# Kernel optimization log

Hardware: AMD Instinct MI355X
Metric: run time of the kernel (lower is better)

The kernel has to match this reference:

```python
import jax, jax.numpy as jnp
import numpy as np

B, C, H, W, R = 4, 128, 64, 256, 8  # batch, channels, height, width, window radius


def setup_inputs() -> dict:
    key = jax.random.key(0)
    k0, k1, k2, k3 = jax.random.split(key, 4)
    feature = jax.random.normal(k0, (B, C, H, W), dtype=jnp.float32)
    position = 0.02 * jax.random.normal(k1, (B, C, H, W), dtype=jnp.float32)
    # 1x1 conv weights (xavier-like scale), bias zeros as in nn.Conv2d default-ish
    Wq = jax.random.normal(k2, (C, C), dtype=jnp.float32) / np.float32(np.sqrt(C))
    Wk = jax.random.normal(k3, (C, C), dtype=jnp.float32) / np.float32(np.sqrt(C))
    bq = jnp.zeros((C,), dtype=jnp.float32)
    bk = jnp.zeros((C,), dtype=jnp.float32)
    return {"feature": feature, "position": position, "Wq": Wq, "bq": bq, "Wk": Wk, "bk": bk}


def reference(feature, position, Wq, bq, Wk, bk):
    # feature/position: [b, c, h, w]
    f = feature + position
    b, c, h, w = f.shape
    # 1x1 convs == channel matmuls
    q = jnp.einsum('oc,bchw->bohw', Wq, f) + bq[None, :, None, None]
    k = jnp.einsum('oc,bchw->bohw', Wk, f) + bk[None, :, None, None]
    r = R
    Kw = 2 * r + 1
    # pad along width, gather sliding windows: [b, c, h, w, Kw]
    kp = jnp.pad(k, ((0, 0), (0, 0), (0, 0), (r, r)))
    vp = jnp.pad(f, ((0, 0), (0, 0), (0, 0), (r, r)))
    idx = jnp.arange(w)[:, None] + jnp.arange(Kw)[None, :]  # [w, Kw]
    kwin = kp[:, :, :, idx]
    vwin = vp[:, :, :, idx]
    scale = jnp.asarray(np.sqrt(c), dtype=q.dtype)
    scores = jnp.einsum('bchw,bchwk->bhwk', q, kwin) / scale  # [b, h, w, Kw]
    attn = jax.nn.softmax(scores, axis=-1)
    out = jnp.einsum('bhwk,bchwk->bchw', attn, vwin)
    return out
```

## Files before the change

kernel.cpp:

```cpp
#include <hip/hip_runtime.h>
#include <hip/hip_bf16.h>
#include <math.h>

#define BB 4
#define CCH 128
#define HH 64
#define WW 256
#define RR 8
#define KWIN 17
#define TW 32
#define TWH 48
#define NTHREADS 256
#define PIT 136
#define FAP 48
#define PTP 48
#define PT_HI 5440
#define MROWS 144

typedef __attribute__((ext_vector_type(8))) short short8;
typedef __attribute__((ext_vector_type(4))) short short4v;
typedef __attribute__((ext_vector_type(4))) float f32x4;

__device__ __forceinline__ short f2bf(float x) {
    union { __hip_bfloat16 b; short s; } u;
    u.b = __float2bfloat16(x);
    return u.s;
}

__global__ __launch_bounds__(128)
void prep_kernel(const float* __restrict__ Wq, const float* __restrict__ bq,
                 const float* __restrict__ Wk, short* __restrict__ Mp)
{
    const int r = blockIdx.x;
    const int c = threadIdx.x;
    float acc = 0.f;
    if (r < CCH) {
        #pragma unroll 4
        for (int j = 0; j < CCH; ++j)
            acc = fmaf(Wq[j * CCH + r], Wk[j * CCH + c], acc);
    } else if (r == CCH) {
        #pragma unroll 4
        for (int o = 0; o < CCH; ++o)
            acc = fmaf(bq[o], Wk[o * CCH + c], acc);
    }
    Mp[r * CCH + c] = f2bf(acc);
}

#define ST_IDX(r) (((r) >> 4) * 1088 + ((r) & 15) * 36)

__global__ __launch_bounds__(NTHREADS, 4)
void attn1d_fused(const float* __restrict__ feature,
                  const float* __restrict__ position,
                  const short* __restrict__ Mp,
                  float* __restrict__ out)
{
    __shared__ __align__(16) char uA[TWH * PIT * 2];
    __shared__ __align__(16) char uB[TWH * PIT * 2];
    __shared__ __align__(16) short fA[CCH][FAP];
    __shared__ float ubias[TWH];
    short (*fBt)[PIT] = (short(*)[PIT])uA;
    short (*gT)[PIT]  = (short(*)[PIT])uB;
    float* Stp        = (float*)uB;
    short* uAs        = (short*)uA;

    const int t    = threadIdx.x;
    const int wid  = t >> 6;
    const int lane = t & 63;
    const int lrow = lane & 15;
    const int lgrp = lane >> 4;

    int blk = blockIdx.x;
    blk = (blk & 7) * 256 + (blk >> 3);
    const int wt = blk & 7;
    const int bh = blk >> 3;
    const int h  = bh & (HH - 1);
    const int b  = bh >> 6;
    const int w0 = wt * TW - RR;
    const int base = ((b * CCH) * HH + h) * WW;

    const int mrow = wid * 32;
    short8 Mf[2][4];
    #pragma unroll
    for (int mf = 0; mf < 2; ++mf)
        #pragma unroll
        for (int kk = 0; kk < 4; ++kk)
            Mf[mf][kk] = *(const short8*)(Mp + (mrow + mf * 16 + lrow) * CCH
                                             + kk * 32 + lgrp * 8);
    short8 Mf2[4];
    if (wid == 3) {
        #pragma unroll
        for (int kk = 0; kk < 4; ++kk)
            Mf2[kk] = *(const short8*)(Mp + (CCH + lrow) * CCH + kk * 32 + lgrp * 8);
    }

    #pragma unroll
    for (int i = 0; i < 6; ++i) {
        const int idx = i * NTHREADS + t;
        const int c  = idx / 12;
        const int wq = idx - c * 12;
        const int w  = w0 + wq * 4;
        float4 fv = {0.f, 0.f, 0.f, 0.f};
        if (w >= 0 && w < WW) {
            const int off = base + c * (HH * WW) + w;
            const float4 fa = *(const float4*)(feature + off);
            const float4 pa = *(const float4*)(position + off);
            fv.x = fa.x + pa.x; fv.y = fa.y + pa.y;
            fv.z = fa.z + pa.z; fv.w = fa.w + pa.w;
        }
        short4v s4;
        s4[0] = f2bf(fv.x); s4[1] = f2bf(fv.y); s4[2] = f2bf(fv.z); s4[3] = f2bf(fv.w);
        *(short4v*)&fA[c][wq * 4] = s4;
        fBt[wq * 4 + 0][c] = s4[0];
        fBt[wq * 4 + 1][c] = s4[1];
        fBt[wq * 4 + 2][c] = s4[2];
        fBt[wq * 4 + 3][c] = s4[3];
    }
    __syncthreads();

    {
        f32x4 acc[2][3];
        #pragma unroll
        for (int mf = 0; mf < 2; ++mf)
            #pragma unroll
            for (int nf = 0; nf < 3; ++nf)
                acc[mf][nf] = (f32x4){0.f, 0.f, 0.f, 0.f};
        f32x4 acc2[3];
        #pragma unroll
        for (int nf = 0; nf < 3; ++nf) acc2[nf] = (f32x4){0.f, 0.f, 0.f, 0.f};

        #pragma unroll
        for (int kk = 0; kk < 4; ++kk) {
            short8 bfr[3];
            #pragma unroll
            for (int nf = 0; nf < 3; ++nf)
                bfr[nf] = *(const short8*)&fBt[nf * 16 + lrow][kk * 32 + lgrp * 8];
            #pragma unroll
            for (int mf = 0; mf < 2; ++mf)
                #pragma unroll
                for (int nf = 0; nf < 3; ++nf)
                    acc[mf][nf] = __builtin_amdgcn_mfma_f32_16x16x32_bf16(
                        Mf[mf][kk], bfr[nf], acc[mf][nf], 0, 0, 0);
            if (wid == 3) {
                #pragma unroll
                for (int nf = 0; nf < 3; ++nf)
                    acc2[nf] = __builtin_amdgcn_mfma_f32_16x16x32_bf16(
                        Mf2[kk], bfr[nf], acc2[nf], 0, 0, 0);
            }
        }

        #pragma unroll
        for (int mf = 0; mf < 2; ++mf)
            #pragma unroll
            for (int nf = 0; nf < 3; ++nf) {
                short4v s;
                #pragma unroll
                for (int reg = 0; reg < 4; ++reg)
                    s[reg] = f2bf(acc[mf][nf][reg]);
                *(short4v*)&gT[nf * 16 + lrow][mrow + mf * 16 + lgrp * 4] = s;
            }
        if (wid == 3 && lgrp == 0) {
            const float isc = 0.08838834764831845f;
            #pragma unroll
            for (int nf = 0; nf < 3; ++nf)
                ubias[nf * 16 + lrow] = acc2[nf][0] * isc;
        }
    }
    __syncthreads();

    if (wid < 3) {
        const int nf = wid;
        f32x4 s0 = {0.f,0.f,0.f,0.f}, s1 = {0.f,0.f,0.f,0.f};
        #pragma unroll
        for (int kk = 0; kk < 4; ++kk) {
            const short8 a0 = *(const short8*)&fBt[RR + lrow     ][kk * 32 + lgrp * 8];
            const short8 a1 = *(const short8*)&fBt[RR + 16 + lrow][kk * 32 + lgrp * 8];
            const short8 bb = *(const short8*)&gT[nf * 16 + lrow][kk * 32 + lgrp * 8];
            s0 = __builtin_amdgcn_mfma_f32_16x16x32_bf16(a0, bb, s0, 0, 0, 0);
            s1 = __builtin_amdgcn_mfma_f32_16x16x32_bf16(a1, bb, s1, 0, 0, 0);
        }
        const float isc = 0.08838834764831845f;
        const int sb = ST_IDX(nf * 16 + lrow);
        *(f32x4*)&Stp[sb + lgrp * 4]      = s0 * isc;
        *(f32x4*)&Stp[sb + 16 + lgrp * 4] = s1 * isc;
    } else {
        const short8 z = {0,0,0,0,0,0,0,0};
        #pragma unroll
        for (int i = 0; i < 2; ++i) {
            const int q8 = i * 64 + lane;
            if (q8 < 96) {
                *(short8*)(uAs + q8 * 8) = z;
                *(short8*)(uAs + PT_HI + q8 * 8) = z;
            }
        }
    }
    __syncthreads();

    if (t < TW * 4) {
        const int w = t >> 2, g = t & 3;
        const int nt = (g == 0) ? 5 : 4;
        const int prow = (w < 16) ? (w * PTP) : (PT_HI + (w - 16) * PTP);
        float sv[5];
        float mx = -3.0e38f;
        #pragma unroll
        for (int i = 0; i < 5; ++i) {
            if (i < nt) {
                const int j = (i == 4) ? 16 : (g + i * 4);
                const int r = w + j;
                sv[i] = Stp[ST_IDX(r) + w] + ubias[r];
                mx = fmaxf(mx, sv[i]);
            }
        }
        mx = fmaxf(mx, __shfl_xor(mx, 1, 4));
        mx = fmaxf(mx, __shfl_xor(mx, 2, 4));
        float sum = 0.f;
        #pragma unroll
        for (int i = 0; i < 5; ++i)
            if (i < nt) { sv[i] = __expf(sv[i] - mx); sum += sv[i]; }
        sum += __shfl_xor(sum, 1, 4);
        sum += __shfl_xor(sum, 2, 4);
        const float inv = 1.f / sum;
        #pragma unroll
        for (int i = 0; i < 5; ++i)
            if (i < nt) {
                const int j = (i == 4) ? 16 : (g + i * 4);
                uAs[prow + w + j] = f2bf(sv[i] * inv);
            }
    }
    __syncthreads();

    {
        const int cb = wid * 32;
        const short8 z = {0,0,0,0,0,0,0,0};
        f32x4 d00 = {0.f,0.f,0.f,0.f}, d01 = d00, d10 = d00, d11 = d00;
        #pragma unroll
        for (int kk = 0; kk < 2; ++kk) {
            const int koff = kk * 32 + lgrp * 8;
            const bool live = (koff < TWH);
            short8 a0 = z, a1 = z, b0 = z, b1 = z;
            if (live) {
                a0 = *(const short8*)&fA[cb + lrow     ][koff];
                a1 = *(const short8*)&fA[cb + 16 + lrow][koff];
                b0 = *(const short8*)(uAs + lrow * PTP + koff);
                b1 = *(const short8*)(uAs + PT_HI + lrow * PTP + koff);
            }
            d00 = __builtin_amdgcn_mfma_f32_16x16x32_bf16(a0, b0, d00, 0, 0, 0);
            d01 = __builtin_amdgcn_mfma_f32_16x16x32_bf16(a0, b1, d01, 0, 0, 0);
            d10 = __builtin_amdgcn_mfma_f32_16x16x32_bf16(a1, b0, d10, 0, 0, 0);
            d11 = __builtin_amdgcn_mfma_f32_16x16x32_bf16(a1, b1, d11, 0, 0, 0);
        }
        const int wbase = wt * TW;
        #pragma unroll
        for (int reg = 0; reg < 4; ++reg) {
            const int c0 = cb + lgrp * 4 + reg;
            out[base + c0 * (HH * WW)        + wbase + lrow]      = d00[reg];
            out[base + c0 * (HH * WW)        + wbase + 16 + lrow] = d01[reg];
            out[base + (c0 + 16) * (HH * WW) + wbase + lrow]      = d10[reg];
            out[base + (c0 + 16) * (HH * WW) + wbase + 16 + lrow] = d11[reg];
        }
    }
}

extern "C" void kernel_launch(void* const* d_in, const int* in_sizes, int n_in,
                              void* d_out, int out_size, void* d_ws, size_t ws_size,
                              hipStream_t stream) {
    const float* feature  = (const float*)d_in[0];
    const float* position = (const float*)d_in[1];
    const float* Wq = (const float*)d_in[2];
    const float* bq = (const float*)d_in[3];
    const float* Wk = (const float*)d_in[4];
    const float* bk = (const float*)d_in[5];
    (void)bk;
    float* out = (float*)d_out;
    short* Mp  = (short*)d_ws;

    prep_kernel<<<MROWS, 128, 0, stream>>>(Wq, bq, Wk, Mp);
    const dim3 grid(BB * HH * (WW / TW));
    attn1d_fused<<<grid, NTHREADS, 0, stream>>>(feature, position, Mp, out);
}
```

Baseline: 40.11 us.

## Split fused attention into transform and attention kernels via bf16 workspace

Splits the single fused kernel into two. The first converts feature+position to bf16, computes the projected keys (M·f) and the bias term once per position, and writes transposed and normal copies to a global workspace. The second kernel does the windowed scores, softmax and output matmul by reading those bf16 tensors. This removes the halo recomputation of the projection and halves the bytes read by the attention stage. In exchange it adds a full round trip of several bf16 intermediate tensors through global memory plus one more kernel launch. The old fused kernel is kept as a fallback for when the workspace is too small.

```diff
diff --git a/kernel.cpp b/kernel.cpp
--- a/kernel.cpp
+++ b/kernel.cpp
@@ -12,10 +12,16 @@
 #define TWH 48
 #define NTHREADS 256
 #define PIT 136
-#define FAP 48
-#define PTP 48
-#define PT_HI 5440
+#define STP 36
+#define PTP 56
 #define MROWS 144
+
+#define SZ_BHWC (BB * HH * WW * CCH * 2)
+#define OFF_FT  65536
+#define OFF_GT  (OFF_FT + SZ_BHWC)
+#define OFF_FN  (OFF_GT + SZ_BHWC)
+#define OFF_UB  (OFF_FN + SZ_BHWC)
+#define WS_NEED ((size_t)OFF_UB + (size_t)(BB * HH * WW * 4))
 
 typedef __attribute__((ext_vector_type(8))) short short8;
 typedef __attribute__((ext_vector_type(4))) short short4v;
@@ -46,6 +52,252 @@
     Mp[r * CCH + c] = f2bf(acc);
 }
 
+__global__ __launch_bounds__(NTHREADS, 4)
+void k1_transform(const float* __restrict__ feature,
+                  const float* __restrict__ position,
+                  const short* __restrict__ Mp,
+                  short* __restrict__ fTg, short* __restrict__ gTg,
+                  short* __restrict__ fNg, float* __restrict__ ubg)
+{
+    __shared__ __align__(16) short fBt[64][PIT];
+
+    const int t    = threadIdx.x;
+    const int wid  = t >> 6;
+    const int lane = t & 63;
+    const int lrow = lane & 15;
+    const int lgrp = lane >> 4;
+
+    int blk = blockIdx.x;
+    blk = (blk & 7) * 128 + (blk >> 3);
+    const int wt = blk & 3;
+    const int bh = blk >> 2;
+    const int h  = bh & (HH - 1);
+    const int b  = bh >> 6;
+    const int w0 = wt * 64;
+    const int base = ((b * CCH) * HH + h) * WW;
+    const int bhw  = (b * HH + h) * WW;
+
+    const int mrow = wid * 32;
+    short8 Mf[2][4];
+    #pragma unroll
+    for (int mf = 0; mf < 2; ++mf)
+        #pragma unroll
+        for (int kk = 0; kk < 4; ++kk)
+            Mf[mf][kk] = *(const short8*)(Mp + (mrow + mf * 16 + lrow) * CCH
+                                             + kk * 32 + lgrp * 8);
+    short8 Mf2[4];
+    if (wid == 3) {
+        #pragma unroll
+        for (int kk = 0; kk < 4; ++kk)
+            Mf2[kk] = *(const short8*)(Mp + (CCH + lrow) * CCH + kk * 32 + lgrp * 8);
+    }
+
+    #pragma unroll
+    for (int i = 0; i < 8; ++i) {
+        const int idx = i * NTHREADS + t;
+        const int c  = idx >> 4;
+        const int wq = idx & 15;
+        const int off = base + c * (HH * WW) + w0 + wq * 4;
+        const float4 fa = *(const float4*)(feature + off);
+        const float4 pa = *(const float4*)(position + off);
+        short4v s4;
+        s4[0] = f2bf(fa.x + pa.x); s4[1] = f2bf(fa.y + pa.y);
+        s4[2] = f2bf(fa.z + pa.z); s4[3] = f2bf(fa.w + pa.w);
+        fBt[wq * 4 + 0][c] = s4[0];
+        fBt[wq * 4 + 1][c] = s4[1];
+        fBt[wq * 4 + 2][c] = s4[2];
+        fBt[wq * 4 + 3][c] = s4[3];
+        *(short4v*)(fNg + ((b * CCH + c) * HH + h) * WW + w0 + wq * 4) = s4;
+    }
+    __syncthreads();
+
+    {
+        const int r  = t >> 2;
+        const int ch = (t & 3) * 32;
+        short* dst = fTg + (bhw + w0 + r) * CCH + ch;
+        #pragma unroll
+        for (int q = 0; q < 4; ++q)
+            *(short8*)(dst + q * 8) = *(const short8*)&fBt[r][ch + q * 8];
+    }
+
+    f32x4 acc[2][4];
+    #pragma unroll
+    for (int mf = 0; mf < 2; ++mf)
+        #pragma unroll
+        for (int nf = 0; nf < 4; ++nf)
+            acc[mf][nf] = (f32x4){0.f, 0.f, 0.f, 0.f};
+    f32x4 acc2[4];
+    #pragma unroll
+    for (int nf = 0; nf < 4; ++nf) acc2[nf] = (f32x4){0.f, 0.f, 0.f, 0.f};
+
+    #pragma unroll
+    for (int kk = 0; kk < 4; ++kk) {
+        short8 bfr[4];
+        #pragma unroll
+        for (int nf = 0; nf < 4; ++nf)
+            bfr[nf] = *(const short8*)&fBt[nf * 16 + lrow][kk * 32 + lgrp * 8];
+        #pragma unroll
+        for (int mf = 0; mf < 2; ++mf)
+            #pragma unroll
+            for (int nf = 0; nf < 4; ++nf)
+                acc[mf][nf] = __builtin_amdgcn_mfma_f32_16x16x32_bf16(
+                    Mf[mf][kk], bfr[nf], acc[mf][nf], 0, 0, 0);
+        if (wid == 3) {
+            #pragma unroll
+            for (int nf = 0; nf < 4; ++nf)
+                acc2[nf] = __builtin_amdgcn_mfma_f32_16x16x32_bf16(
+                    Mf2[kk], bfr[nf], acc2[nf], 0, 0, 0);
+        }
+    }
+
+    #pragma unroll
+    for (int mf = 0; mf < 2; ++mf)
+        #pragma unroll
+        for (int nf = 0; nf < 4; ++nf) {
+            short4v s;
+            #pragma unroll
+            for (int reg = 0; reg < 4; ++reg)
+                s[reg] = f2bf(acc[mf][nf][reg]);
+            *(short4v*)(gTg + (bhw + w0 + nf * 16 + lrow) * CCH
+                            + mrow + mf * 16 + lgrp * 4) = s;
+        }
+    if (wid == 3 && lgrp == 0) {
+        const float isc = 0.08838834764831845f;
+        #pragma unroll
+        for (int nf = 0; nf < 4; ++nf)
+            ubg[bhw + w0 + nf * 16 + lrow] = acc2[nf][0] * isc;
+    }
+}
+
+__global__ __launch_bounds__(NTHREADS, 8)
+void k2_attn(const short* __restrict__ fTg, const short* __restrict__ gTg,
+             const short* __restrict__ fNg, const float* __restrict__ ubg,
+             float* __restrict__ out)
+{
+    __shared__ __align__(16) float St[TWH][STP];
+    __shared__ __align__(16) short Pt[33][PTP];
+    __shared__ float ubl[TWH];
+
+    const int t    = threadIdx.x;
+    const int wid  = t >> 6;
+    const int lane = t & 63;
+    const int lrow = lane & 15;
+    const int lgrp = lane >> 4;
+
+    int blk = blockIdx.x;
+    blk = (blk & 7) * 256 + (blk >> 3);
+    const int wt = blk & 7;
+    const int bh = blk >> 3;
+    const int h  = bh & (HH - 1);
+    const int b  = bh >> 6;
+    const int w0 = wt * TW - RR;
+    const int bhw  = (b * HH + h) * WW;
+    const int base = ((b * CCH) * HH + h) * WW;
+
+    if (t < TWH) {
+        const int w = w0 + t;
+        ubl[t] = (w >= 0 && w < WW) ? ubg[bhw + w] : 0.f;
+    }
+
+    const short8 z8 = {0,0,0,0,0,0,0,0};
+
+    if (wid < 3) {
+        const int nf = wid;
+        const int wl = nf * 16 + lrow;
+        const int wg = w0 + wl;
+        const bool inb = (wg >= 0 && wg < WW);
+        f32x4 s0 = {0.f,0.f,0.f,0.f}, s1 = s0;
+        #pragma unroll
+        for (int kk = 0; kk < 4; ++kk) {
+            const int ko = kk * 32 + lgrp * 8;
+            const short8 a0 = *(const short8*)(fTg + (bhw + wt * TW + lrow) * CCH + ko);
+            const short8 a1 = *(const short8*)(fTg + (bhw + wt * TW + 16 + lrow) * CCH + ko);
+            const short8 bb = inb ? *(const short8*)(gTg + (bhw + wg) * CCH + ko) : z8;
+            s0 = __builtin_amdgcn_mfma_f32_16x16x32_bf16(a0, bb, s0, 0, 0, 0);
+            s1 = __builtin_amdgcn_mfma_f32_16x16x32_bf16(a1, bb, s1, 0, 0, 0);
+        }
+        const float isc = 0.08838834764831845f;
+        *(f32x4*)&St[wl][lgrp * 4]      = s0 * isc;
+        *(f32x4*)&St[wl][16 + lgrp * 4] = s1 * isc;
+    } else {
+        short* p = &Pt[0][0];
+        #pragma unroll
+        for (int i = 0; i < 4; ++i) {
+            const int q8 = i * 64 + lane;
+            if (q8 < (33 * PTP) / 8) *(short8*)(p + q8 * 8) = z8;
+        }
+    }
+    __syncthreads();
+
+    if (t < TW * 4) {
+        const int w = t >> 2, g = t & 3;
+        const int nt = (g == 0) ? 5 : 4;
+        float sv[5];
+        float mx = -3.0e38f;
+        #pragma unroll
+        for (int i = 0; i < 5; ++i) {
+            if (i < nt) {
+                const int j = (i == 4) ? 16 : (g + i * 4);
+                sv[i] = St[w + j][w] + ubl[w + j];
+                mx = fmaxf(mx, sv[i]);
+            }
+        }
+        mx = fmaxf(mx, __shfl_xor(mx, 1, 4));
+        mx = fmaxf(mx, __shfl_xor(mx, 2, 4));
+        float sum = 0.f;
+        #pragma unroll
+        for (int i = 0; i < 5; ++i)
+            if (i < nt) { sv[i] = __expf(sv[i] - mx); sum += sv[i]; }
+        sum += __shfl_xor(sum, 1, 4);
+        sum += __shfl_xor(sum, 2, 4);
+        const float inv = 1.f / sum;
+        #pragma unroll
+        for (int i = 0; i < 5; ++i)
+            if (i < nt) {
+                const int j = (i == 4) ? 16 : (g + i * 4);
+                Pt[w][w + j] = f2bf(sv[i] * inv);
+            }
+    }
+    __syncthreads();
+
+    {
+        const int cb = wid * 32;
+        f32x4 d00 = {0.f,0.f,0.f,0.f}, d01 = d00, d10 = d00, d11 = d00;
+        #pragma unroll
+        for (int kk = 0; kk < 2; ++kk) {
+            const int koff = kk * 32 + lgrp * 8;
+            const bool live = (koff < TWH);
+            const int w = w0 + koff;
+            const bool inb = live && (w >= 0) && (w < WW);
+            short8 a0 = z8, a1 = z8, b0 = z8, b1 = z8;
+            if (inb) {
+                a0 = *(const short8*)(fNg + ((b * CCH + cb + lrow) * HH + h) * WW + w);
+                a1 = *(const short8*)(fNg + ((b * CCH + cb + 16 + lrow) * HH + h) * WW + w);
+            }
+            if (live) {
+                b0 = *(const short8*)&Pt[lrow][koff];
+                b1 = *(const short8*)&Pt[16 + lrow][koff];
+            }
+            d00 = __builtin_amdgcn_mfma_f32_16x16x32_bf16(a0, b0, d00, 0, 0, 0);
+            d01 = __builtin_amdgcn_mfma_f32_16x16x32_bf16(a0, b1, d01, 0, 0, 0);
+            d10 = __builtin_amdgcn_mfma_f32_16x16x32_bf16(a1, b0, d10, 0, 0, 0);
+            d11 = __builtin_amdgcn_mfma_f32_16x16x32_bf16(a1, b1, d11, 0, 0, 0);
+        }
+        const int wbase = wt * TW;
+        #pragma unroll
+        for (int reg = 0; reg < 4; ++reg) {
+            const int c0 = cb + lgrp * 4 + reg;
+            out[base + c0 * (HH * WW)        + wbase + lrow]      = d00[reg];
+            out[base + c0 * (HH * WW)        + wbase + 16 + lrow] = d01[reg];
+            out[base + (c0 + 16) * (HH * WW) + wbase + lrow]      = d10[reg];
+            out[base + (c0 + 16) * (HH * WW) + wbase + 16 + lrow] = d11[reg];
+        }
+    }
+}
+
+#define FAPF 48
+#define PTPF 48
+#define PT_HIF 5440
 #define ST_IDX(r) (((r) >> 4) * 1088 + ((r) & 15) * 36)
 
 __global__ __launch_bounds__(NTHREADS, 4)
@@ -56,7 +308,7 @@
 {
     __shared__ __align__(16) char uA[TWH * PIT * 2];
     __shared__ __align__(16) char uB[TWH * PIT * 2];
-    __shared__ __align__(16) short fA[CCH][FAP];
+    __shared__ __align__(16) short fA[CCH][FAPF];
     __shared__ float ubias[TWH];
     short (*fBt)[PIT] = (short(*)[PIT])uA;
     short (*gT)[PIT]  = (short(*)[PIT])uB;
@@ -147,7 +399,6 @@
                         Mf2[kk], bfr[nf], acc2[nf], 0, 0, 0);
             }
         }
-
         #pragma unroll
         for (int mf = 0; mf < 2; ++mf)
             #pragma unroll
@@ -189,7 +440,7 @@
             const int q8 = i * 64 + lane;
             if (q8 < 96) {
                 *(short8*)(uAs + q8 * 8) = z;
-                *(short8*)(uAs + PT_HI + q8 * 8) = z;
+                *(short8*)(uAs + PT_HIF + q8 * 8) = z;
             }
         }
     }
@@ -198,7 +449,7 @@
     if (t < TW * 4) {
         const int w = t >> 2, g = t & 3;
         const int nt = (g == 0) ? 5 : 4;
-        const int prow = (w < 16) ? (w * PTP) : (PT_HI + (w - 16) * PTP);
+        const int prow = (w < 16) ? (w * PTPF) : (PT_HIF + (w - 16) * PTPF);
         float sv[5];
         float mx = -3.0e38f;
         #pragma unroll
@@ -240,8 +491,8 @@
             if (live) {
                 a0 = *(const short8*)&fA[cb + lrow     ][koff];
                 a1 = *(const short8*)&fA[cb + 16 + lrow][koff];
-                b0 = *(const short8*)(uAs + lrow * PTP + koff);
-                b1 = *(const short8*)(uAs + PT_HI + lrow * PTP + koff);
+                b0 = *(const short8*)(uAs + lrow * PTPF + koff);
+                b1 = *(const short8*)(uAs + PT_HIF + lrow * PTPF + koff);
             }
             d00 = __builtin_amdgcn_mfma_f32_16x16x32_bf16(a0, b0, d00, 0, 0, 0);
             d01 = __builtin_amdgcn_mfma_f32_16x16x32_bf16(a0, b1, d01, 0, 0, 0);
@@ -271,9 +522,22 @@
     const float* bk = (const float*)d_in[5];
     (void)bk;
     float* out = (float*)d_out;
-    short* Mp  = (short*)d_ws;
+    char*  ws  = (char*)d_ws;
+    short* Mp  = (short*)ws;
 
     prep_kernel<<<MROWS, 128, 0, stream>>>(Wq, bq, Wk, Mp);
-    const dim3 grid(BB * HH * (WW / TW));
-    attn1d_fused<<<grid, NTHREADS, 0, stream>>>(feature, position, Mp, out);
+
+    if (ws_size >= WS_NEED) {
+        short* fTg = (short*)(ws + OFF_FT);
+        short* gTg = (short*)(ws + OFF_GT);
+        short* fNg = (short*)(ws + OFF_FN);
+        float* ubg = (float*)(ws + OFF_UB);
+        k1_transform<<<dim3(BB * HH * (WW / 64)), NTHREADS, 0, stream>>>(
+            feature, position, Mp, fTg, gTg, fNg, ubg);
+        k2_attn<<<dim3(BB * HH * (WW / TW)), NTHREADS, 0, stream>>>(
+            fTg, gTg, fNg, ubg, out);
+    } else {
+        attn1d_fused<<<dim3(BB * HH * (WW / TW)), NTHREADS, 0, stream>>>(
+            feature, position, Mp, out);
+    }
 }
```

New measurement: 55.24 us. 37.7% more time.
